# Kernel tuning notes

Hardware: AMD Instinct MI355X
Metric: run time of the kernel (lower is better)

## Reference

```python
import jax, jax.numpy as jnp
import numpy as np

B = 1024
N_ATOMS = 51
FLAT = 7 * 7 * 64  # conv output: 84->20->9->7 spatial, 64 channels


def _conv(x, w, b, s):
    # x: NCHW, w: OIHW, VALID padding, stride s
    y = jax.lax.conv_general_dilated(
        x, w, window_strides=(s, s), padding='VALID',
        dimension_numbers=('NCHW', 'OIHW', 'NCHW'))
    return y + b[None, :, None, None]


def setup_inputs() -> dict:
    key = jax.random.key(0)
    ks = jax.random.split(key, 8)

    def w(k, shape, fan_in):
        return jax.random.normal(k, shape, dtype=jnp.float32) / np.float32(np.sqrt(fan_in))

    return {
        'x': jax.random.uniform(ks[0], (B, 4, 84, 84), jnp.float32, 0.0, 256.0),
        'cw1': w(ks[1], (32, 4, 8, 8), 4 * 8 * 8), 'cb1': jnp.zeros((32,), jnp.float32),
        'cw2': w(ks[2], (64, 32, 4, 4), 32 * 4 * 4), 'cb2': jnp.zeros((64,), jnp.float32),
        'cw3': w(ks[3], (64, 64, 3, 3), 64 * 3 * 3), 'cb3': jnp.zeros((64,), jnp.float32),
        'fw1': w(ks[4], (FLAT, 256), FLAT), 'fb1': jnp.zeros((256,), jnp.float32),
        'fw2': w(ks[5], (256, N_ATOMS), 256), 'fb2': jnp.zeros((N_ATOMS,), jnp.float32),
        'z': jnp.linspace(-10.0, 10.0, N_ATOMS).astype(jnp.float32),  # support atoms
        'n_out': 6,
    }


def reference(x, cw1, cb1, cw2, cb2, cw3, cb3, fw1, fb1, fw2, fb2, z, n_out):
    x = x / 256.0
    x = jax.nn.relu(_conv(x, cw1, cb1, 4))  # [B,32,20,20]
    x = jax.nn.relu(_conv(x, cw2, cb2, 2))  # [B,64,9,9]
    x = jax.nn.relu(_conv(x, cw3, cb3, 1))  # [B,64,7,7]
    h = x.reshape(x.shape[0], -1)           # [B,3136]
    h = jax.nn.relu(h @ fw1 + fb1)          # [B,256]
    p = jax.nn.softmax(h @ fw2 + fb2, axis=1)  # [B,n_atoms]
    # Original loop writes fc_layers(x)[i] identically for every action j:
    dist = jnp.broadcast_to(p[:, None, :], (p.shape[0], n_out, p.shape[1]))
    res = jnp.einsum('bna,a->bn', dist, z)  # expected value per action
    return (dist, res)
```

## Files before the change

### kernel.cpp

```cpp
#include <hip/hip_runtime.h>
#include <hip/hip_fp16.h>

#define RL(x) __builtin_amdgcn_readfirstlane(x)

typedef _Float16 f16x8 __attribute__((ext_vector_type(8)));
typedef _Float16 f16x4 __attribute__((ext_vector_type(4)));
typedef float    f32x16 __attribute__((ext_vector_type(16)));

__global__ __launch_bounds__(256) void wprep_k(const float* __restrict__ w1,
                                               const float* __restrict__ w2,
                                               const float* __restrict__ w3,
                                               __half* __restrict__ w1h,
                                               __half* __restrict__ w2h,
                                               __half* __restrict__ w3h) {
  int i = blockIdx.x * 256 + threadIdx.x;
  if (i < 8192) {
    int kx = i & 7, oc = (i >> 3) & 31, ky = (i >> 8) & 7, ic = i >> 11;
    w1h[i] = __float2half(w1[oc * 256 + ic * 64 + ky * 8 + kx] * 0.00390625f);
  }
  if (i < 32768) {
    int j = i & 7, ln = (i >> 3) & 31, kh = (i >> 8) & 1, ot = (i >> 9) & 1, ic = i >> 10;
    int k = kh * 8 + j, kx = k >> 2, ky = k & 3, oc = ot * 32 + ln;
    w2h[i] = __float2half(w2[oc * 512 + ic * 16 + ky * 4 + kx]);
  }
  if (i < 65536) {
    int j = i & 7, ln = (i >> 3) & 31, kh = (i >> 8) & 1, ot = (i >> 9) & 1, ic = i >> 10;
    int k = kh * 8 + j, kx = k >> 2, ky = k & 3, oc = ot * 32 + ln;
    float v = (kx < 3 && ky < 3) ? w3[oc * 576 + ic * 9 + ky * 3 + kx] : 0.f;
    w3h[i] = __float2half(v);
  }
}

__global__ __launch_bounds__(256, 2) void conv1_k(const float* __restrict__ x,
                                                  const __half* __restrict__ w1h,
                                                  const float* __restrict__ bias,
                                                  __half* __restrict__ out) {
  const int b = blockIdx.x;
  const int tid = threadIdx.x;
  const int lane = tid & 63;
  const int wv   = RL(tid >> 6);
  const int kh = lane >> 5;
  const int ln = lane & 31;
  const int nt = (wv == 0) ? 4 : 3;

  int ibs[4], pvv[4];
#pragma unroll
  for (int tt = 0; tt < 4; ++tt) {
    int p = (wv + tt * 4) * 32 + ln;
    pvv[tt] = (p < 400);
    if (p > 399) p = 399;
    int py = p / 20, px = p - py * 20;
    ibs[tt] = py * 336 + px * 4;
  }

  f32x16 acc[4];
#pragma unroll
  for (int tt = 0; tt < 4; ++tt)
#pragma unroll
    for (int r = 0; r < 16; ++r) acc[tt][r] = 0.f;

  const float* xb = x + b * 28224;

#pragma unroll 1
  for (int ic = 0; ic < 4; ++ic) {
#pragma unroll
    for (int t = 0; t < 4; ++t) {
      f16x8 aw = *(const f16x8*)(w1h + ((ic * 8 + 2 * t + kh) * 32 + ln) * 8);
      const float* rp = xb + ic * 7056 + (2 * t + kh) * 84;
#pragma unroll
      for (int tt = 0; tt < 4; ++tt) {
        if (tt < nt) {
          const float* ap = rp + ibs[tt];
          float4 lo = *(const float4*)ap;
          float4 hi = *(const float4*)(ap + 4);
          __half2 p0 = __floats2half2_rn(lo.x, lo.y);
          __half2 p1 = __floats2half2_rn(lo.z, lo.w);
          __half2 p2 = __floats2half2_rn(hi.x, hi.y);
          __half2 p3 = __floats2half2_rn(hi.z, hi.w);
          uint4 u = make_uint4(*(unsigned*)&p0, *(unsigned*)&p1,
                               *(unsigned*)&p2, *(unsigned*)&p3);
          f16x8 bx = *(f16x8*)&u;
          acc[tt] = __builtin_amdgcn_mfma_f32_32x32x16_f16(aw, bx, acc[tt], 0, 0, 0);
        }
      }
    }
  }

  float bv[16];
#pragma unroll
  for (int r = 0; r < 16; ++r)
    bv[r] = bias[(r & 3) + 8 * (r >> 2) + 4 * kh];

#pragma unroll
  for (int tt = 0; tt < 4; ++tt) {
    if (tt < nt && pvv[tt]) {
      const int p = (wv + tt * 4) * 32 + ln;
#pragma unroll
      for (int r = 0; r < 16; ++r) {
        const int oc = (r & 3) + 8 * (r >> 2) + 4 * kh;
        float v = acc[tt][r] + bv[r];
        out[b * 12800 + oc * 400 + p] = __float2half(v > 0.f ? v : 0.f);
      }
    }
  }
}

__global__ __launch_bounds__(256) void t1_k(const __half* __restrict__ in,
                                            __half* __restrict__ out) {
  __shared__ __half t[64][65];
  const int kb = blockIdx.x * 64;
  const int bb = blockIdx.y * 64;
  const int lane = threadIdx.x & 63;
  const int ty   = threadIdx.x >> 6;
#pragma unroll
  for (int r = ty; r < 64; r += 4)
    t[r][lane] = in[(bb + r) * 12800 + kb + lane];
  __syncthreads();
#pragma unroll
  for (int r = ty; r < 64; r += 4)
    out[(kb + r) * 1024 + bb + lane] = t[lane][r];
}

__global__ __launch_bounds__(256, 1) void conv2_k(const __half* __restrict__ in,
                                                  const __half* __restrict__ w2h,
                                                  const float* __restrict__ bias,
                                                  __half* __restrict__ out) {
  __shared__ __align__(16) __half sh[2][9216];
  const int bid = blockIdx.x;
  const int opy = bid % 9;
  const int bt  = bid / 9;
  const int bbase = bt * 64;
  const int tid  = threadIdx.x;
  const int lane = tid & 63;
  const int wv   = RL(tid >> 6);
  const int octile = wv & 1;
  const int bsub   = wv >> 1;
  const int kh = lane >> 5;
  const int ln = lane & 31;

  const unsigned short* inu = (const unsigned short*)in;
  const unsigned short* wu  = (const unsigned short*)w2h;

  int roff[5], offA[5];
#pragma unroll
  for (int p = 0; p < 5; ++p) {
    int idx = p * 256 + tid;
    int px = idx >> 6, b = idx & 63;
    roff[p] = px * 1024 + b;
    offA[p] = b * 128 + ((((px >> 1) ^ (b & 7)) << 3) | ((px & 1) << 2));
  }
  const int base0 = (40 * opy) * 1024 + bbase;

  f32x16 acc[9];
#pragma unroll
  for (int ox = 0; ox < 9; ++ox)
#pragma unroll
    for (int r = 0; r < 16; ++r) acc[ox][r] = 0.f;

  ushort4 s0, s1, s2, s3, s4; uint2 sW;

#define C2_LOAD(icv) do {                                                     \
    const unsigned short* ibp = inu + (icv) * 409600 + base0;                 \
    s0 = make_ushort4(ibp[roff[0]], ibp[roff[0]+20480], ibp[roff[0]+40960], ibp[roff[0]+61440]); \
    s1 = make_ushort4(ibp[roff[1]], ibp[roff[1]+20480], ibp[roff[1]+40960], ibp[roff[1]+61440]); \
    s2 = make_ushort4(ibp[roff[2]], ibp[roff[2]+20480], ibp[roff[2]+40960], ibp[roff[2]+61440]); \
    s3 = make_ushort4(ibp[roff[3]], ibp[roff[3]+20480], ibp[roff[3]+40960], ibp[roff[3]+61440]); \
    s4 = make_ushort4(ibp[roff[4]], ibp[roff[4]+20480], ibp[roff[4]+40960], ibp[roff[4]+61440]); \
    sW = *(const uint2*)(wu + (icv) * 1024 + tid * 4);                        \
  } while (0)

#define C2_STORE(buf) do {                                                    \
    *(uint2*)&sh[buf][offA[0]] = make_uint2((unsigned)s0.x | ((unsigned)s0.y << 16), (unsigned)s0.z | ((unsigned)s0.w << 16)); \
    *(uint2*)&sh[buf][offA[1]] = make_uint2((unsigned)s1.x | ((unsigned)s1.y << 16), (unsigned)s1.z | ((unsigned)s1.w << 16)); \
    *(uint2*)&sh[buf][offA[2]] = make_uint2((unsigned)s2.x | ((unsigned)s2.y << 16), (unsigned)s2.z | ((unsigned)s2.w << 16)); \
    *(uint2*)&sh[buf][offA[3]] = make_uint2((unsigned)s3.x | ((unsigned)s3.y << 16), (unsigned)s3.z | ((unsigned)s3.w << 16)); \
    *(uint2*)&sh[buf][offA[4]] = make_uint2((unsigned)s4.x | ((unsigned)s4.y << 16), (unsigned)s4.z | ((unsigned)s4.w << 16)); \
    *(uint2*)&sh[buf][8192 + tid * 4] = sW;                                   \
  } while (0)

  const int offW = 8192 + octile * 512 + kh * 256 + ln * 8;
  const int bloc = bsub * 32 + ln;
  const int bx7  = bloc & 7;
  const int brow = bloc * 128;

  int cur = 0;
  C2_LOAD(0);
#pragma unroll 1
  for (int ic = 0; ic < 32; ++ic) {
    __syncthreads();
    C2_STORE(cur);
    const int icn = ic < 31 ? ic + 1 : 31;
    C2_LOAD(icn);
    __syncthreads();
    f16x8 aw = *(const f16x8*)&sh[cur][offW];
#pragma unroll
    for (int ox = 0; ox < 9; ++ox) {
      f16x8 bx = *(const f16x8*)&sh[cur][brow + (((ox + kh) ^ bx7) << 3)];
      acc[ox] = __builtin_amdgcn_mfma_f32_32x32x16_f16(aw, bx, acc[ox], 0, 0, 0);
    }
    cur ^= 1;
  }
#undef C2_LOAD
#undef C2_STORE

  float bv[16];
#pragma unroll
  for (int r = 0; r < 16; ++r)
    bv[r] = bias[octile * 32 + (r & 3) + 8 * (r >> 2) + 4 * kh];
  const int bout = bbase + bloc;
#pragma unroll
  for (int ox = 0; ox < 9; ++ox) {
#pragma unroll
    for (int r = 0; r < 16; ++r) {
      const int oc = octile * 32 + (r & 3) + 8 * (r >> 2) + 4 * kh;
      float v = acc[ox][r] + bv[r];
      out[(oc * 81 + opy * 9 + ox) * 1024 + bout] = __float2half(v > 0.f ? v : 0.f);
    }
  }
}

__global__ __launch_bounds__(256, 1) void conv3_k(const __half* __restrict__ in,
                                                  const __half* __restrict__ w3h,
                                                  const float* __restrict__ bias,
                                                  __half* __restrict__ out) {
  __shared__ __align__(16) __half sh[2][3840];
  const int bid = blockIdx.x;
  const int opy = bid % 7;
  const int bt  = bid / 7;
  const int bbase = bt * 64;
  const int tid  = threadIdx.x;
  const int lane = tid & 63;
  const int wv   = RL(tid >> 6);
  const int octile = wv & 1;
  const int bsub   = wv >> 1;
  const int kh = lane >> 5;
  const int ln = lane & 31;

  const unsigned short* inu = (const unsigned short*)in;
  const unsigned short* wu  = (const unsigned short*)w3h;

  int rof[4];
#pragma unroll
  for (int ky = 0; ky < 4; ++ky) {
    int r = opy + ky; if (r > 8) r = 8;
    rof[ky] = r * 9 * 1024;
  }
  int gof[3], sof[3];
#pragma unroll
  for (int p = 0; p < 3; ++p) {
    int idx = p * 256 + tid;
    int b = idx & 63, px = idx >> 6;
    int pxc = px > 8 ? 8 : px;
    gof[p] = pxc * 1024 + bbase + b;
    sof[p] = b * 44 + px * 4;
  }

  f32x16 acc[7];
#pragma unroll
  for (int ox = 0; ox < 7; ++ox)
#pragma unroll
    for (int r = 0; r < 16; ++r) acc[ox][r] = 0.f;

  ushort4 s0, s1, s2; uint2 sW;

#define C3_LOAD(icv) do {                                                     \
    const unsigned short* ibp = inu + (icv) * 82944;                          \
    s0 = make_ushort4(ibp[rof[0]+gof[0]], ibp[rof[1]+gof[0]],                 \
                      ibp[rof[2]+gof[0]], ibp[rof[3]+gof[0]]);                \
    s1 = make_ushort4(ibp[rof[0]+gof[1]], ibp[rof[1]+gof[1]],                 \
                      ibp[rof[2]+gof[1]], ibp[rof[3]+gof[1]]);                \
    if (tid < 128)                                                            \
      s2 = make_ushort4(ibp[rof[0]+gof[2]], ibp[rof[1]+gof[2]],               \
                        ibp[rof[2]+gof[2]], ibp[rof[3]+gof[2]]);              \
    sW = *(const uint2*)(wu + (icv) * 1024 + tid * 4);                        \
  } while (0)

#define C3_STORE(buf) do {                                                    \
    *(uint2*)&sh[buf][sof[0]] = make_uint2((unsigned)s0.x | ((unsigned)s0.y << 16), (unsigned)s0.z | ((unsigned)s0.w << 16)); \
    *(uint2*)&sh[buf][sof[1]] = make_uint2((unsigned)s1.x | ((unsigned)s1.y << 16), (unsigned)s1.z | ((unsigned)s1.w << 16)); \
    if (tid < 128)                                                            \
      *(uint2*)&sh[buf][sof[2]] = make_uint2((unsigned)s2.x | ((unsigned)s2.y << 16), (unsigned)s2.z | ((unsigned)s2.w << 16)); \
    *(uint2*)&sh[buf][2816 + tid * 4] = sW;                                   \
  } while (0)

  const int offW = 2816 + octile * 512 + kh * 256 + ln * 8;
  const int bloc = bsub * 32 + ln;
  const int brow = bloc * 44;

  int cur = 0;
  C3_LOAD(0);
#pragma unroll 1
  for (int ic = 0; ic < 64; ++ic) {
    __syncthreads();
    C3_STORE(cur);
    const int icn = ic < 63 ? ic + 1 : 63;
    C3_LOAD(icn);
    __syncthreads();
    f16x8 aw = *(const f16x8*)&sh[cur][offW];
#pragma unroll
    for (int ox = 0; ox < 7; ++ox) {
      const int p0 = ox + 2 * kh;
      f16x4 lo = *(const f16x4*)&sh[cur][brow + p0 * 4];
      f16x4 hi = *(const f16x4*)&sh[cur][brow + p0 * 4 + 4];
      f16x8 bx;
      bx[0]=lo[0]; bx[1]=lo[1]; bx[2]=lo[2]; bx[3]=lo[3];
      bx[4]=hi[0]; bx[5]=hi[1]; bx[6]=hi[2]; bx[7]=hi[3];
      acc[ox] = __builtin_amdgcn_mfma_f32_32x32x16_f16(aw, bx, acc[ox], 0, 0, 0);
    }
    cur ^= 1;
  }
#undef C3_LOAD
#undef C3_STORE

  float bv[16];
#pragma unroll
  for (int r = 0; r < 16; ++r)
    bv[r] = bias[octile * 32 + (r & 3) + 8 * (r >> 2) + 4 * kh];
  const int bout = bbase + bloc;
#pragma unroll
  for (int ox = 0; ox < 7; ++ox) {
#pragma unroll
    for (int r = 0; r < 16; ++r) {
      const int oc = octile * 32 + (r & 3) + 8 * (r >> 2) + 4 * kh;
      float v = acc[ox][r] + bv[r];
      out[(oc * 49 + opy * 7 + ox) * 1024 + bout] = __float2half(v > 0.f ? v : 0.f);
    }
  }
}

__global__ __launch_bounds__(64, 2) void fc1a_k(const __half* __restrict__ a,
                                                const float* __restrict__ w,
                                                float* __restrict__ part) {
  const int bid = blockIdx.x;
  const int jg  = (bid >> 3) & 15;
  const int grp = ((bid >> 7) << 3) | (bid & 7);
  const int kc  = grp & 15;
  const int bg  = grp >> 4;
  const int lane = threadIdx.x;

  float acc[16];
#pragma unroll
  for (int j = 0; j < 16; ++j) acc[j] = 0.f;

  const __half* ap = a + kc * 196 * 1024 + bg * 64 + lane;
  const float* wp0 = w + kc * 196 * 256 + jg * 16;

#pragma unroll 4
  for (int k = 0; k < 196; ++k) {
    float av = __half2float(ap[k * 1024]);
    const float* wp = wp0 + k * 256;
#pragma unroll
    for (int j = 0; j < 16; ++j) acc[j] = fmaf(av, wp[j], acc[j]);
  }
#pragma unroll
  for (int j = 0; j < 16; ++j)
    part[(kc * 256 + jg * 16 + j) * 1024 + bg * 64 + lane] = acc[j];
}

__global__ __launch_bounds__(256) void fc1b_k(const float* __restrict__ part,
                                              const float* __restrict__ bias,
                                              float* __restrict__ h) {
  int idx = blockIdx.x * 256 + threadIdx.x;
  float s = bias[idx >> 10];
#pragma unroll
  for (int c = 0; c < 16; ++c) s += part[c * 262144 + idx];
  h[idx] = s > 0.f ? s : 0.f;
}

__global__ __launch_bounds__(256) void fc2_k(const float* __restrict__ h,
                                             const float* __restrict__ w,
                                             const float* __restrict__ bias,
                                             const float* __restrict__ z,
                                             float* __restrict__ dist,
                                             float* __restrict__ res) {
  __shared__ float wl[256 * 51];
  const int tid = threadIdx.x;
#pragma unroll
  for (int i = tid; i < 256 * 51; i += 256) wl[i] = w[i];
  __syncthreads();

  const int j   = tid & 63;
  const int b   = blockIdx.x * 4 + RL(tid >> 6);
  const int jc = j < 51 ? j : 50;
  float acc = bias[jc];
#pragma unroll 8
  for (int k = 0; k < 256; ++k)
    acc = fmaf(h[k * 1024 + b], wl[k * 51 + jc], acc);
  float logit = (j < 51) ? acc : -1e30f;
  float m = logit;
#pragma unroll
  for (int o = 32; o > 0; o >>= 1) m = fmaxf(m, __shfl_xor(m, o, 64));
  float e = (j < 51) ? __expf(logit - m) : 0.f;
  float ssum = e;
#pragma unroll
  for (int o = 32; o > 0; o >>= 1) ssum += __shfl_xor(ssum, o, 64);
  float p = e / ssum;
  float zv = (j < 51) ? z[jc] : 0.f;
  float rz = p * zv;
#pragma unroll
  for (int o = 32; o > 0; o >>= 1) rz += __shfl_xor(rz, o, 64);
  if (j < 51) {
    float* db = dist + b * 6 * 51 + j;
#pragma unroll
    for (int n = 0; n < 6; ++n) db[n * 51] = p;
  }
  if (j < 6) res[b * 6 + j] = rz;
}

extern "C" void kernel_launch(void* const* d_in, const int* in_sizes, int n_in,
                              void* d_out, int out_size, void* d_ws, size_t ws_size,
                              hipStream_t stream) {
  const float* x   = (const float*)d_in[0];
  const float* cw1 = (const float*)d_in[1];
  const float* cb1 = (const float*)d_in[2];
  const float* cw2 = (const float*)d_in[3];
  const float* cb2 = (const float*)d_in[4];
  const float* cw3 = (const float*)d_in[5];
  const float* cb3 = (const float*)d_in[6];
  const float* fw1 = (const float*)d_in[7];
  const float* fb1 = (const float*)d_in[8];
  const float* fw2 = (const float*)d_in[9];
  const float* fb2 = (const float*)d_in[10];
  const float* z   = (const float*)d_in[11];

  float* ws = (float*)d_ws;
  __half* c1h = (__half*)ws;
  __half* c1t = (__half*)(ws + 6553600);
  __half* c2t = (__half*)(ws + 13107200);
  __half* c3t = (__half*)(ws + 15761408);
  float*  pw  = ws;
  float*  h_t = ws + 4194304;

  __half* w3h  = (__half*)d_out;
  __half* w1h  = (__half*)((float*)d_out + 36864);
  __half* w2h  = (__half*)((float*)d_out + 45056);

  float* dist = (float*)d_out;
  float* res  = dist + 1024 * 6 * 51;

  wprep_k<<<256, 256, 0, stream>>>(cw1, cw2, cw3, w1h, w2h, w3h);
  conv1_k<<<1024, 256, 0, stream>>>(x, w1h, cb1, c1h);
  t1_k<<<dim3(200, 16), 256, 0, stream>>>(c1h, c1t);
  conv2_k<<<144, 256, 0, stream>>>(c1t, w2h, cb2, c2t);
  conv3_k<<<112, 256, 0, stream>>>(c2t, w3h, cb3, c3t);
  fc1a_k<<<4096, 64, 0, stream>>>(c3t, fw1, pw);
  fc1b_k<<<1024, 256, 0, stream>>>(pw, fb1, h_t);
  fc2_k<<<256, 256, 0, stream>>>(h_t, fw2, fb2, z, dist, res);
}
```

Baseline: 366.1 us.

## Stage conv1 input through double-buffered LDS as fp16 and preload weights

Conv1 now loads each input channel plane once with coalesced float4 loads, converts it to fp16 and writes it into a double-buffered shared-memory tile with a padded row stride. The MFMA operands are then read from LDS instead of issuing overlapping global loads per output tile. All 16 weight fragments are hoisted into registers before the loop. This cuts redundant global traffic and conversion work but adds two barriers per channel, about 29KB of LDS and extra registers, which may reduce occupancy.

```diff
diff --git a/kernel.cpp b/kernel.cpp
--- a/kernel.cpp
+++ b/kernel.cpp
@@ -35,6 +35,7 @@
                                                   const __half* __restrict__ w1h,
                                                   const float* __restrict__ bias,
                                                   __half* __restrict__ out) {
+  __shared__ __align__(16) __half xs[2][7392];
   const int b = blockIdx.x;
   const int tid = threadIdx.x;
   const int lane = tid & 63;
@@ -43,14 +44,32 @@
   const int ln = lane & 31;
   const int nt = (wv == 0) ? 4 : 3;
 
-  int ibs[4], pvv[4];
+  int lof[4], pvv[4];
 #pragma unroll
   for (int tt = 0; tt < 4; ++tt) {
     int p = (wv + tt * 4) * 32 + ln;
     pvv[tt] = (p < 400);
     if (p > 399) p = 399;
     int py = p / 20, px = p - py * 20;
-    ibs[tt] = py * 336 + px * 4;
+    lof[tt] = py * 4 * 88 + px * 4;
+  }
+
+  int goff[7], soff[7], gok[7];
+#pragma unroll
+  for (int p = 0; p < 7; ++p) {
+    int idx = p * 256 + tid;
+    gok[p] = (idx < 1764);
+    if (idx > 1763) idx = 1763;
+    int row = idx / 21, c4 = idx - row * 21;
+    goff[p] = idx * 4;
+    soff[p] = row * 88 + c4 * 4;
+  }
+
+  f16x8 wreg[16];
+#pragma unroll
+  for (int f = 0; f < 16; ++f) {
+    const int ic = f >> 2, t = f & 3;
+    wreg[f] = *(const f16x8*)(w1h + ((ic * 8 + 2 * t + kh) * 32 + ln) * 8);
   }
 
   f32x16 acc[4];
@@ -60,31 +79,52 @@
     for (int r = 0; r < 16; ++r) acc[tt][r] = 0.f;
 
   const float* xb = x + b * 28224;
-
+  float4 g[7];
+
+#define C1_LOAD(icv) do {                                                     \
+    const float* xp = xb + (icv) * 7056;                                      \
+    _Pragma("unroll") for (int p = 0; p < 7; ++p)                             \
+      if (gok[p]) g[p] = *(const float4*)(xp + goff[p]);                      \
+  } while (0)
+
+#define C1_STORE(buf) do {                                                    \
+    _Pragma("unroll") for (int p = 0; p < 7; ++p)                             \
+      if (gok[p]) {                                                           \
+        __half2 h01 = __floats2half2_rn(g[p].x, g[p].y);                      \
+        __half2 h23 = __floats2half2_rn(g[p].z, g[p].w);                      \
+        *(uint2*)&xs[buf][soff[p]] =                                          \
+            make_uint2(*(unsigned*)&h01, *(unsigned*)&h23);                   \
+      }                                                                       \
+  } while (0)
+
+  int cur = 0;
+  C1_LOAD(0);
 #pragma unroll 1
   for (int ic = 0; ic < 4; ++ic) {
+    __syncthreads();
+    C1_STORE(cur);
+    if (ic < 3) C1_LOAD(ic + 1);
+    __syncthreads();
 #pragma unroll
     for (int t = 0; t < 4; ++t) {
-      f16x8 aw = *(const f16x8*)(w1h + ((ic * 8 + 2 * t + kh) * 32 + ln) * 8);
-      const float* rp = xb + ic * 7056 + (2 * t + kh) * 84;
+      const int rb = (2 * t + kh) * 88;
+      const f16x8 aw = wreg[ic * 4 + t];
 #pragma unroll
       for (int tt = 0; tt < 4; ++tt) {
         if (tt < nt) {
-          const float* ap = rp + ibs[tt];
-          float4 lo = *(const float4*)ap;
-          float4 hi = *(const float4*)(ap + 4);
-          __half2 p0 = __floats2half2_rn(lo.x, lo.y);
-          __half2 p1 = __floats2half2_rn(lo.z, lo.w);
-          __half2 p2 = __floats2half2_rn(hi.x, hi.y);
-          __half2 p3 = __floats2half2_rn(hi.z, hi.w);
-          uint4 u = make_uint4(*(unsigned*)&p0, *(unsigned*)&p1,
-                               *(unsigned*)&p2, *(unsigned*)&p3);
-          f16x8 bx = *(f16x8*)&u;
+          f16x4 lo = *(const f16x4*)&xs[cur][rb + lof[tt]];
+          f16x4 hi = *(const f16x4*)&xs[cur][rb + lof[tt] + 4];
+          f16x8 bx;
+          bx[0]=lo[0]; bx[1]=lo[1]; bx[2]=lo[2]; bx[3]=lo[3];
+          bx[4]=hi[0]; bx[5]=hi[1]; bx[6]=hi[2]; bx[7]=hi[3];
           acc[tt] = __builtin_amdgcn_mfma_f32_32x32x16_f16(aw, bx, acc[tt], 0, 0, 0);
         }
       }
     }
-  }
+    cur ^= 1;
+  }
+#undef C1_LOAD
+#undef C1_STORE
 
   float bv[16];
 #pragma unroll
```

Measured after the change: 376.0 us. 1.03x slower.
